# Optimization experiments

Measured on AMD Instinct MI355X. Metric: run time of the kernel, lower is better.

The kernel has to match this reference:

```python
import jax, jax.numpy as jnp
import numpy as np

EPS = 1e-5  # BatchNorm2d default eps
HEAD_DIM = 64


def conv1x1_bn_silu(x, w, gamma, beta, mean, var):
    # x: [B, Cin, H, W], w: [Cout, Cin] (1x1 conv, no bias)
    y = jnp.einsum('oc,bchw->bohw', w, x)
    scale = (gamma / jnp.sqrt(var + EPS))[None, :, None, None]
    shift = (beta - mean * gamma / jnp.sqrt(var + EPS))[None, :, None, None]
    y = y * scale + shift
    return y * jax.nn.sigmoid(y)  # SiLU


def setup_inputs() -> dict:
    key = jax.random.key(0)
    ks = jax.random.split(key, 11)
    B, C, H, W = 4, 256, 64, 64
    C3 = 3 * C
    return {
        'x': jax.random.normal(ks[0], (B, C, H, W), jnp.float32),
        'qkv_w': jax.random.normal(ks[1], (C3, C), jnp.float32) * (1.0 / np.sqrt(C)),
        'qkv_gamma': jax.random.uniform(ks[2], (C3,), jnp.float32, 0.5, 1.5),
        'qkv_beta': jax.random.normal(ks[3], (C3,), jnp.float32) * 0.1,
        'qkv_mean': jax.random.normal(ks[4], (C3,), jnp.float32) * 0.1,
        'qkv_var': jax.random.uniform(ks[5], (C3,), jnp.float32, 0.5, 1.5),
        'proj_w': jax.random.normal(ks[6], (C, C), jnp.float32) * (1.0 / np.sqrt(C)),
        'proj_gamma': jax.random.uniform(ks[7], (C,), jnp.float32, 0.5, 1.5),
        'proj_beta': jax.random.normal(ks[8], (C,), jnp.float32) * 0.1,
        'proj_mean': jax.random.normal(ks[9], (C,), jnp.float32) * 0.1,
        'proj_var': jax.random.uniform(ks[10], (C,), jnp.float32, 0.5, 1.5),
    }


def reference(x, qkv_w, qkv_gamma, qkv_beta, qkv_mean, qkv_var,
              proj_w, proj_gamma, proj_beta, proj_mean, proj_var):
    B, C, H, W = x.shape
    hd = HEAD_DIM
    nh = C // hd
    scale = hd ** -0.5

    qkv = conv1x1_bn_silu(x, qkv_w, qkv_gamma, qkv_beta, qkv_mean, qkv_var)
    # [B, 3C, H, W] -> [B, 3, nh, hd, HW] -> (3, B, nh, HW, hd)
    qkv = qkv.reshape(B, 3, nh, hd, H * W).transpose(1, 0, 2, 4, 3)
    q, k, v = qkv[0], qkv[1], qkv[2]  # each [B, nh, HW, hd]

    attn = jnp.einsum('bhqd,bhkd->bhqk', q, k) * scale
    attn = jax.nn.softmax(attn, axis=-1)
    out = jnp.einsum('bhqk,bhkd->bhqd', attn, v)  # [B, nh, HW, hd]
    out = out.transpose(0, 1, 3, 2).reshape(B, C, H, W)

    return conv1x1_bn_silu(out, proj_w, proj_gamma, proj_beta, proj_mean, proj_var)
```

## Files before the change

kernel.cpp:

```cpp
#include <hip/hip_runtime.h>
#include <hip/hip_bf16.h>
#include <math.h>

#define SLEN 4096
#define CIN 256
#define C3 768
#define NH 4
#define HD 64
#define BATCH 4

typedef __attribute__((ext_vector_type(8))) short bf16x8;
typedef __attribute__((ext_vector_type(4))) float f32x4;
typedef __attribute__((ext_vector_type(16))) float f32x16;

__device__ __forceinline__ short f2bf(float f) {
    union { float f; unsigned u; } v; v.f = f;
    unsigned r = v.u + 0x7fff + ((v.u >> 16) & 1);
    return (short)(r >> 16);
}

__device__ __forceinline__ unsigned cvt_pk(float lo, float hi) {
    unsigned r;
    asm("v_cvt_pk_bf16_f32 %0, %1, %2" : "=v"(r) : "v"(lo), "v"(hi));
    return r;
}

__global__ void k_convert_w(const float* __restrict__ qkvw, const float* __restrict__ projw,
                            short* __restrict__ qkvw_bf, short* __restrict__ projw_bf) {
    int i = blockIdx.x * 256 + threadIdx.x;
    if (i < C3 * CIN) qkvw_bf[i] = f2bf(qkvw[i]);
    if (i < CIN * CIN) projw_bf[i] = f2bf(projw[i]);
}

__global__ void k_transpose_x(const float* __restrict__ x, short* __restrict__ xT) {
    __shared__ float t[32][33];
    int b = blockIdx.z;
    int c0 = blockIdx.y * 32, s0 = blockIdx.x * 32;
    int tid = threadIdx.x;
    int r = tid >> 3, c4 = (tid & 7) * 4;
    const float* src = x + ((size_t)b * CIN + c0 + r) * SLEN + s0 + c4;
    float4 v = *reinterpret_cast<const float4*>(src);
    t[r][c4 + 0] = v.x; t[r][c4 + 1] = v.y; t[r][c4 + 2] = v.z; t[r][c4 + 3] = v.w;
    __syncthreads();
    int s_r = tid >> 3, cc = (tid & 7) * 4;
    short4 o = make_short4(f2bf(t[cc + 0][s_r]), f2bf(t[cc + 1][s_r]),
                           f2bf(t[cc + 2][s_r]), f2bf(t[cc + 3][s_r]));
    *reinterpret_cast<short4*>(xT + ((size_t)b * SLEN + s0 + s_r) * CIN + c0 + cc) = o;
}

__launch_bounds__(256)
__global__ void k_qkv(const short* __restrict__ xT, const short* __restrict__ wbf,
                      const float* __restrict__ g, const float* __restrict__ be,
                      const float* __restrict__ mu, const float* __restrict__ va,
                      short* __restrict__ Q, short* __restrict__ Kb, short* __restrict__ Vt) {
    int wv = threadIdx.x >> 6, l = threadIdx.x & 63, lr = l & 15, lg = l >> 4;
    int b = blockIdx.z;
    int s0 = blockIdx.x * 128 + wv * 32;
    int o0 = blockIdx.y * 64;
    f32x4 acc[2][4] = {};
    const short* aptr = xT + ((size_t)b * SLEN + s0 + lr) * CIN + lg * 8;
    const short* bptr = wbf + (size_t)(o0 + lr) * CIN + lg * 8;
#pragma unroll
    for (int k0 = 0; k0 < CIN; k0 += 32) {
        bf16x8 a0 = *(const bf16x8*)(aptr + k0);
        bf16x8 a1 = *(const bf16x8*)(aptr + 16 * CIN + k0);
#pragma unroll
        for (int oj = 0; oj < 4; oj++) {
            bf16x8 bb = *(const bf16x8*)(bptr + oj * 16 * CIN + k0);
            acc[0][oj] = __builtin_amdgcn_mfma_f32_16x16x32_bf16(a0, bb, acc[0][oj], 0, 0, 0);
            acc[1][oj] = __builtin_amdgcn_mfma_f32_16x16x32_bf16(a1, bb, acc[1][oj], 0, 0, 0);
        }
    }
    int which = o0 >> 8;
    int h = (o0 & 255) >> 6;
    int bh = b * NH + h;
    const float QSC = 0.125f * 1.44269504088896f;
#pragma unroll
    for (int oj = 0; oj < 4; oj++) {
        int o = o0 + oj * 16 + lr;
        float sc = g[o] * rsqrtf(va[o] + 1e-5f);
        float sh = be[o] - mu[o] * sc;
        int d = o & 63;
#pragma unroll
        for (int qi = 0; qi < 2; qi++) {
#pragma unroll
            for (int i = 0; i < 4; i++) {
                float y = acc[qi][oj][i] * sc + sh;
                float z = y / (1.f + __expf(-y));
                int s = s0 + qi * 16 + lg * 4 + i;
                if (which == 0) {
                    Q[((size_t)bh * SLEN + s) * HD + d] = f2bf(z * QSC);
                } else if (which == 1) {
                    Kb[((size_t)bh * SLEN + s) * HD + d] = f2bf(z);
                } else {
                    Vt[((size_t)bh * HD + d) * SLEN + s] = f2bf(z);
                }
            }
        }
    }
}

__launch_bounds__(256)
__global__ void k_attn(const short* __restrict__ Q, const short* __restrict__ Kg,
                       const short* __restrict__ Vg, short* __restrict__ aout) {
    __shared__ __align__(16) short klds[2][64][64];
    __shared__ __align__(16) short vlds[2][64][64];
    int tid = threadIdx.x;
    int wv = tid >> 6, l = tid & 63;
    int q32 = l & 31;
    int hi  = l >> 5;
    int bh = blockIdx.y;
    int q0 = blockIdx.x * 128 + wv * 32;

    const short* kg = Kg + (size_t)bh * SLEN * HD;
    const short* vg = Vg + (size_t)bh * HD * SLEN;

    bf16x8 qf[4];
    {
        const short* qb = Q + ((size_t)bh * SLEN + q0 + q32) * HD + hi * 8;
        qf[0] = *(const bf16x8*)(qb);
        qf[1] = *(const bf16x8*)(qb + 16);
        qf[2] = *(const bf16x8*)(qb + 32);
        qf[3] = *(const bf16x8*)(qb + 48);
    }

    bf16x8 ones;
#pragma unroll
    for (int e = 0; e < 8; ++e) ones[e] = (short)0x3F80;

    f32x16 oacc0 = {}, oacc1 = {}, sacc = {};
    float mrun = -1e30f;

    int srow = wv * 16 + (l >> 3);
    int gs = l & 7;
    int swcol = (gs ^ (l >> 3)) * 8;
    int4 rK0, rK1, rV0, rV1;

#define LOADREG(t) do { \
    const short* kgt = kg + ((size_t)(t) * 64 + srow) * HD + gs * 8; \
    rK0 = *(const int4*)(kgt); \
    rK1 = *(const int4*)(kgt + 8 * HD); \
    const short* vgt = vg + (size_t)srow * SLEN + (t) * 64 + gs * 8; \
    rV0 = *(const int4*)(vgt); \
    rV1 = *(const int4*)(vgt + 8 * SLEN); \
} while (0)

#define WRITELDS(bufb) do { \
    *(int4*)(&klds[bufb][srow][swcol]) = rK0; \
    *(int4*)(&klds[bufb][srow + 8][swcol]) = rK1; \
    *(int4*)(&vlds[bufb][srow][swcol]) = rV0; \
    *(int4*)(&vlds[bufb][srow + 8][swcol]) = rV1; \
} while (0)

#define BAR() do { asm volatile("" ::: "memory"); __builtin_amdgcn_s_barrier(); asm volatile("" ::: "memory"); } while (0)

    LOADREG(0);
    WRITELDS(0);
    LOADREG(1);
    asm volatile("s_waitcnt lgkmcnt(0)" ::: "memory");
    BAR();

    const int swz = (l & 7) << 4;

    for (int t = 0; t < SLEN / 64; ++t) {
        if (t < SLEN / 64 - 1) {
            WRITELDS((t + 1) & 1);
            if (t + 2 < SLEN / 64) LOADREG(t + 2);
        }

        const short* kb = &klds[t & 1][0][0];
        const short* vb = &vlds[t & 1][0][0];
        const short* krow0 = kb + q32 * 64;
        const short* krow1 = kb + (32 + q32) * 64;

        f32x16 s0v = {}, s1v = {};
#pragma unroll
        for (int jd = 0; jd < 4; ++jd) {
            int col = ((jd * 32 + hi * 16) ^ swz) >> 1;
            bf16x8 k0 = *(const bf16x8*)(krow0 + col);
            bf16x8 k1 = *(const bf16x8*)(krow1 + col);
            s0v = __builtin_amdgcn_mfma_f32_32x32x16_bf16(k0, qf[jd], s0v, 0, 0, 0);
            s1v = __builtin_amdgcn_mfma_f32_32x32x16_bf16(k1, qf[jd], s1v, 0, 0, 0);
        }

        float pm = fmaxf(s0v[0], s0v[1]);
#pragma unroll
        for (int r = 2; r < 16; r += 2) pm = fmaxf(pm, fmaxf(s0v[r], s0v[r + 1]));
#pragma unroll
        for (int r = 0; r < 16; r += 2) pm = fmaxf(pm, fmaxf(s1v[r], s1v[r + 1]));
        pm = fmaxf(pm, __shfl_xor(pm, 32));

        if (!__all(pm <= mrun + 10.0f)) {
            float mn = fmaxf(mrun, pm);
            float al = __builtin_amdgcn_exp2f(mrun - mn);
            mrun = mn;
#pragma unroll
            for (int r = 0; r < 16; ++r) { oacc0[r] *= al; oacc1[r] *= al; }
            sacc[0] *= al;
        }

#pragma unroll
        for (int r = 0; r < 16; ++r) {
            s0v[r] = __builtin_amdgcn_exp2f(s0v[r] - mrun);
            s1v[r] = __builtin_amdgcn_exp2f(s1v[r] - mrun);
        }

        const short* vrow0 = vb + q32 * 64;
        const short* vrow1 = vb + (32 + q32) * 64;
#pragma unroll
        for (int kc = 0; kc < 4; ++kc) {
            const f32x16& sv = (kc < 2) ? s0v : s1v;
            const int base = (kc & 1) * 8;
            unsigned A0 = cvt_pk(sv[base + 0], sv[base + 1]);
            unsigned A1 = cvt_pk(sv[base + 2], sv[base + 3]);
            unsigned A2 = cvt_pk(sv[base + 4], sv[base + 5]);
            unsigned A3 = cvt_pk(sv[base + 6], sv[base + 7]);
            asm volatile("v_permlane32_swap_b32 %0, %1" : "+v"(A0), "+v"(A2));
            asm volatile("v_permlane32_swap_b32 %0, %1" : "+v"(A1), "+v"(A3));
            union { bf16x8 v; unsigned u[4]; } pf;
            pf.u[0] = A0; pf.u[1] = A1; pf.u[2] = A2; pf.u[3] = A3;
            int col = ((kc * 32 + hi * 16) ^ swz) >> 1;
            bf16x8 v0 = *(const bf16x8*)(vrow0 + col);
            bf16x8 v1 = *(const bf16x8*)(vrow1 + col);
            oacc0 = __builtin_amdgcn_mfma_f32_32x32x16_bf16(v0, pf.v, oacc0, 0, 0, 0);
            oacc1 = __builtin_amdgcn_mfma_f32_32x32x16_bf16(v1, pf.v, oacc1, 0, 0, 0);
            sacc  = __builtin_amdgcn_mfma_f32_32x32x16_bf16(ones, pf.v, sacc, 0, 0, 0);
        }

        if (t < SLEN / 64 - 1) {
            asm volatile("s_waitcnt lgkmcnt(0)" ::: "memory");
            BAR();
        }
    }

    float inv = 1.f / sacc[0];
    int b = bh >> 2, h = bh & 3;
    short* ob = aout + ((size_t)b * SLEN + q0 + q32) * CIN + h * HD;
#pragma unroll
    for (int g4 = 0; g4 < 4; ++g4) {
        uint2 st0, st1;
        st0.x = cvt_pk(oacc0[4 * g4 + 0] * inv, oacc0[4 * g4 + 1] * inv);
        st0.y = cvt_pk(oacc0[4 * g4 + 2] * inv, oacc0[4 * g4 + 3] * inv);
        st1.x = cvt_pk(oacc1[4 * g4 + 0] * inv, oacc1[4 * g4 + 1] * inv);
        st1.y = cvt_pk(oacc1[4 * g4 + 2] * inv, oacc1[4 * g4 + 3] * inv);
        *(uint2*)(ob + 8 * g4 + 4 * hi) = st0;
        *(uint2*)(ob + 32 + 8 * g4 + 4 * hi) = st1;
    }
#undef LOADREG
#undef WRITELDS
#undef BAR
}

__launch_bounds__(256)
__global__ void k_proj(const short* __restrict__ aout, const short* __restrict__ wbf,
                       const float* __restrict__ g, const float* __restrict__ be,
                       const float* __restrict__ mu, const float* __restrict__ va,
                       float* __restrict__ out) {
    int wv = threadIdx.x >> 6, l = threadIdx.x & 63, lr = l & 15, lg = l >> 4;
    int b = blockIdx.z;
    int s0 = blockIdx.x * 128 + wv * 32;
    int o0 = blockIdx.y * 64;
    f32x4 acc[2][4] = {};
    const short* aptr = aout + ((size_t)b * SLEN + s0 + lr) * CIN + lg * 8;
    const short* bptr = wbf + (size_t)(o0 + lr) * CIN + lg * 8;
#pragma unroll
    for (int k0 = 0; k0 < CIN; k0 += 32) {
        bf16x8 a0 = *(const bf16x8*)(aptr + k0);
        bf16x8 a1 = *(const bf16x8*)(aptr + 16 * CIN + k0);
#pragma unroll
        for (int oj = 0; oj < 4; oj++) {
            bf16x8 bb = *(const bf16x8*)(bptr + oj * 16 * CIN + k0);
            acc[0][oj] = __builtin_amdgcn_mfma_f32_16x16x32_bf16(a0, bb, acc[0][oj], 0, 0, 0);
            acc[1][oj] = __builtin_amdgcn_mfma_f32_16x16x32_bf16(a1, bb, acc[1][oj], 0, 0, 0);
        }
    }
#pragma unroll
    for (int oj = 0; oj < 4; oj++) {
        int o = o0 + oj * 16 + lr;
        float sc = g[o] * rsqrtf(va[o] + 1e-5f);
        float sh = be[o] - mu[o] * sc;
#pragma unroll
        for (int qi = 0; qi < 2; qi++) {
            float4 st;
            float* stp = &st.x;
#pragma unroll
            for (int i = 0; i < 4; i++) {
                float y = acc[qi][oj][i] * sc + sh;
                stp[i] = y / (1.f + __expf(-y));
            }
            int s = s0 + qi * 16 + lg * 4;
            *reinterpret_cast<float4*>(out + ((size_t)b * CIN + o) * SLEN + s) = st;
        }
    }
}

extern "C" void kernel_launch(void* const* d_in, const int* in_sizes, int n_in,
                              void* d_out, int out_size, void* d_ws, size_t ws_size,
                              hipStream_t stream) {
    const float* x    = (const float*)d_in[0];
    const float* qkvw = (const float*)d_in[1];
    const float* qg   = (const float*)d_in[2];
    const float* qbe  = (const float*)d_in[3];
    const float* qmu  = (const float*)d_in[4];
    const float* qva  = (const float*)d_in[5];
    const float* pw   = (const float*)d_in[6];
    const float* pg   = (const float*)d_in[7];
    const float* pbe  = (const float*)d_in[8];
    const float* pmu  = (const float*)d_in[9];
    const float* pva  = (const float*)d_in[10];
    float* out = (float*)d_out;

    char* ws = (char*)d_ws;
    short* xT       = (short*)(ws);
    short* qkvw_bf  = (short*)(ws + 8388608);
    short* projw_bf = (short*)(ws + 8781824);
    short* Qb       = (short*)(ws + 8912896);
    short* Kb       = (short*)(ws + 17301504);
    short* Vt       = (short*)(ws + 25690112);
    short* aout     = (short*)(ws + 34078720);

    k_convert_w<<<768, 256, 0, stream>>>(qkvw, pw, qkvw_bf, projw_bf);
    k_transpose_x<<<dim3(128, 8, 4), 256, 0, stream>>>(x, xT);
    k_qkv<<<dim3(32, 12, 4), 256, 0, stream>>>(xT, qkvw_bf, qg, qbe, qmu, qva, Qb, Kb, Vt);
    k_attn<<<dim3(32, 16), 256, 0, stream>>>(Qb, Kb, Vt, aout);
    k_proj<<<dim3(32, 4, 4), 256, 0, stream>>>(aout, projw_bf, pg, pbe, pmu, pva, out);
}
```

Baseline: 173.4 us.

## Software-pipeline attention: overlap next tile's QK^T with current softmax/PV

Restructures the attention main loop so the QK^T MFMAs for tile t+1 are issued alongside the softmax and PV step for tile t, with ping-pong score registers and a 2x-unrolled loop. V gets a triple LDS buffer so the V tile being consumed stays valid while the next one is written. The intent is to hide softmax and exp latency behind matrix-core work. It also adds a launch bound of 2 blocks per SM and a tree-shaped max reduction. The extra live score registers raise VGPR pressure and could cause spills under the occupancy bound.

```diff
diff --git a/kernel.cpp b/kernel.cpp
--- a/kernel.cpp
+++ b/kernel.cpp
@@ -100,11 +100,11 @@
     }
 }
 
-__launch_bounds__(256)
+__launch_bounds__(256, 2)
 __global__ void k_attn(const short* __restrict__ Q, const short* __restrict__ Kg,
                        const short* __restrict__ Vg, short* __restrict__ aout) {
     __shared__ __align__(16) short klds[2][64][64];
-    __shared__ __align__(16) short vlds[2][64][64];
+    __shared__ __align__(16) short vlds[3][64][64];
     int tid = threadIdx.x;
     int wv = tid >> 6, l = tid & 63;
     int q32 = l & 31;
@@ -145,49 +145,43 @@
     rV1 = *(const int4*)(vgt + 8 * SLEN); \
 } while (0)
 
-#define WRITELDS(bufb) do { \
-    *(int4*)(&klds[bufb][srow][swcol]) = rK0; \
-    *(int4*)(&klds[bufb][srow + 8][swcol]) = rK1; \
-    *(int4*)(&vlds[bufb][srow][swcol]) = rV0; \
-    *(int4*)(&vlds[bufb][srow + 8][swcol]) = rV1; \
+#define WRITELDS(kbuf, vbuf) do { \
+    *(int4*)(&klds[kbuf][srow][swcol]) = rK0; \
+    *(int4*)(&klds[kbuf][srow + 8][swcol]) = rK1; \
+    *(int4*)(&vlds[vbuf][srow][swcol]) = rV0; \
+    *(int4*)(&vlds[vbuf][srow + 8][swcol]) = rV1; \
 } while (0)
 
 #define BAR() do { asm volatile("" ::: "memory"); __builtin_amdgcn_s_barrier(); asm volatile("" ::: "memory"); } while (0)
-
-    LOADREG(0);
-    WRITELDS(0);
-    LOADREG(1);
-    asm volatile("s_waitcnt lgkmcnt(0)" ::: "memory");
-    BAR();
+#define WAITBAR() do { asm volatile("s_waitcnt lgkmcnt(0)" ::: "memory"); BAR(); } while (0)
 
     const int swz = (l & 7) << 4;
 
-    for (int t = 0; t < SLEN / 64; ++t) {
-        if (t < SLEN / 64 - 1) {
-            WRITELDS((t + 1) & 1);
-            if (t + 2 < SLEN / 64) LOADREG(t + 2);
-        }
-
+    auto qk = [&](int t, f32x16& d0, f32x16& d1) {
         const short* kb = &klds[t & 1][0][0];
-        const short* vb = &vlds[t & 1][0][0];
         const short* krow0 = kb + q32 * 64;
         const short* krow1 = kb + (32 + q32) * 64;
-
-        f32x16 s0v = {}, s1v = {};
+        d0 = (f32x16){}; d1 = (f32x16){};
 #pragma unroll
         for (int jd = 0; jd < 4; ++jd) {
             int col = ((jd * 32 + hi * 16) ^ swz) >> 1;
             bf16x8 k0 = *(const bf16x8*)(krow0 + col);
             bf16x8 k1 = *(const bf16x8*)(krow1 + col);
-            s0v = __builtin_amdgcn_mfma_f32_32x32x16_bf16(k0, qf[jd], s0v, 0, 0, 0);
-            s1v = __builtin_amdgcn_mfma_f32_32x32x16_bf16(k1, qf[jd], s1v, 0, 0, 0);
-        }
-
-        float pm = fmaxf(s0v[0], s0v[1]);
-#pragma unroll
-        for (int r = 2; r < 16; r += 2) pm = fmaxf(pm, fmaxf(s0v[r], s0v[r + 1]));
-#pragma unroll
-        for (int r = 0; r < 16; r += 2) pm = fmaxf(pm, fmaxf(s1v[r], s1v[r + 1]));
+            d0 = __builtin_amdgcn_mfma_f32_32x32x16_bf16(k0, qf[jd], d0, 0, 0, 0);
+            d1 = __builtin_amdgcn_mfma_f32_32x32x16_bf16(k1, qf[jd], d1, 0, 0, 0);
+        }
+    };
+
+    auto smpv = [&](int tt, f32x16& s0v, f32x16& s1v) {
+        float pa = fmaxf(fmaxf(fmaxf(s0v[0], s0v[1]), fmaxf(s0v[2], s0v[3])),
+                         fmaxf(fmaxf(s0v[4], s0v[5]), fmaxf(s0v[6], s0v[7])));
+        float pb = fmaxf(fmaxf(fmaxf(s0v[8], s0v[9]), fmaxf(s0v[10], s0v[11])),
+                         fmaxf(fmaxf(s0v[12], s0v[13]), fmaxf(s0v[14], s0v[15])));
+        float pc = fmaxf(fmaxf(fmaxf(s1v[0], s1v[1]), fmaxf(s1v[2], s1v[3])),
+                         fmaxf(fmaxf(s1v[4], s1v[5]), fmaxf(s1v[6], s1v[7])));
+        float pd = fmaxf(fmaxf(fmaxf(s1v[8], s1v[9]), fmaxf(s1v[10], s1v[11])),
+                         fmaxf(fmaxf(s1v[12], s1v[13]), fmaxf(s1v[14], s1v[15])));
+        float pm = fmaxf(fmaxf(pa, pb), fmaxf(pc, pd));
         pm = fmaxf(pm, __shfl_xor(pm, 32));
 
         if (!__all(pm <= mrun + 10.0f)) {
@@ -205,6 +199,7 @@
             s1v[r] = __builtin_amdgcn_exp2f(s1v[r] - mrun);
         }
 
+        const short* vb = &vlds[tt % 3][0][0];
         const short* vrow0 = vb + q32 * 64;
         const short* vrow1 = vb + (32 + q32) * 64;
 #pragma unroll
@@ -226,12 +221,36 @@
             oacc1 = __builtin_amdgcn_mfma_f32_32x32x16_bf16(v1, pf.v, oacc1, 0, 0, 0);
             sacc  = __builtin_amdgcn_mfma_f32_32x32x16_bf16(ones, pf.v, sacc, 0, 0, 0);
         }
-
-        if (t < SLEN / 64 - 1) {
-            asm volatile("s_waitcnt lgkmcnt(0)" ::: "memory");
-            BAR();
-        }
-    }
+    };
+
+    f32x16 sA0, sA1, sB0, sB1;
+
+    LOADREG(0);
+    WRITELDS(0, 0);
+    LOADREG(1);
+    WAITBAR();
+
+    WRITELDS(1, 1);
+    LOADREG(2);
+    qk(0, sA0, sA1);
+    WAITBAR();
+
+    for (int t = 1; t < 63; t += 2) {
+        WRITELDS((t + 1) & 1, (t + 1) % 3);
+        LOADREG(t + 2);
+        qk(t, sB0, sB1);
+        smpv(t - 1, sA0, sA1);
+        WAITBAR();
+        WRITELDS((t + 2) & 1, (t + 2) % 3);
+        if (t + 3 < 64) LOADREG(t + 3);
+        qk(t + 1, sA0, sA1);
+        smpv(t, sB0, sB1);
+        WAITBAR();
+    }
+
+    qk(63, sB0, sB1);
+    smpv(62, sA0, sA1);
+    smpv(63, sB0, sB1);
 
     float inv = 1.f / sacc[0];
     int b = bh >> 2, h = bh & 3;
@@ -249,6 +268,7 @@
 #undef LOADREG
 #undef WRITELDS
 #undef BAR
+#undef WAITBAR
 }
 
 __launch_bounds__(256)
```

Measured after the change: 167.5 us. -3.4%, faster.

## Software-pipeline QK^T and softmax/PV across tiles with deeper V buffering

Applied to the files above, without the earlier changes.

Restructures the attention loop so the QK^T MFMAs for the next key tile are issued while the current tile's softmax and PV run, using two score register sets and a manually unrolled four-stage schedule. V gets four LDS buffers and K two, and scores are initialised with the negated running max so the subtraction folds into the MFMA accumulator. When the max has not changed, a fast path skips that subtraction. It also requests two blocks per CU via launch bounds. The cost is higher register pressure and more LDS per block, which may limit occupancy.

```diff
diff --git a/kernel.cpp b/kernel.cpp
--- a/kernel.cpp
+++ b/kernel.cpp
@@ -100,11 +100,10 @@
     }
 }
 
-__launch_bounds__(256)
+__launch_bounds__(256, 2)
 __global__ void k_attn(const short* __restrict__ Q, const short* __restrict__ Kg,
                        const short* __restrict__ Vg, short* __restrict__ aout) {
-    __shared__ __align__(16) short klds[2][64][64];
-    __shared__ __align__(16) short vlds[2][64][64];
+    __shared__ __align__(16) char lds[16384 + 32768];
     int tid = threadIdx.x;
     int wv = tid >> 6, l = tid & 63;
     int q32 = l & 31;
@@ -129,109 +128,141 @@
     for (int e = 0; e < 8; ++e) ones[e] = (short)0x3F80;
 
     f32x16 oacc0 = {}, oacc1 = {}, sacc = {};
-    float mrun = -1e30f;
+    float mrun = 0.0f, bA = 0.0f, bB = 0.0f;
 
     int srow = wv * 16 + (l >> 3);
     int gs = l & 7;
-    int swcol = (gs ^ (l >> 3)) * 8;
+    int swz = (l & 7) << 4;
+    int soff = srow * 128 + ((gs ^ (l >> 3)) << 4);
+    int a0 = q32 * 128 + ((0 * 32 + hi * 16) ^ swz);
+    int a1 = q32 * 128 + ((1 * 32 + hi * 16) ^ swz);
+    int a2 = q32 * 128 + ((2 * 32 + hi * 16) ^ swz);
+    int a3 = q32 * 128 + ((3 * 32 + hi * 16) ^ swz);
+
+    int klane = srow * HD + gs * 8;
+    int vlane = srow * SLEN + gs * 8;
     int4 rK0, rK1, rV0, rV1;
 
-#define LOADREG(t) do { \
-    const short* kgt = kg + ((size_t)(t) * 64 + srow) * HD + gs * 8; \
+#define LOADREG(T) do { \
+    const short* kgt = kg + (size_t)(T) * 4096 + klane; \
     rK0 = *(const int4*)(kgt); \
     rK1 = *(const int4*)(kgt + 8 * HD); \
-    const short* vgt = vg + (size_t)srow * SLEN + (t) * 64 + gs * 8; \
+    const short* vgt = vg + (size_t)(T) * 64 + vlane; \
     rV0 = *(const int4*)(vgt); \
     rV1 = *(const int4*)(vgt + 8 * SLEN); \
 } while (0)
 
-#define WRITELDS(bufb) do { \
-    *(int4*)(&klds[bufb][srow][swcol]) = rK0; \
-    *(int4*)(&klds[bufb][srow + 8][swcol]) = rK1; \
-    *(int4*)(&vlds[bufb][srow][swcol]) = rV0; \
-    *(int4*)(&vlds[bufb][srow + 8][swcol]) = rV1; \
+#define WRITELDS(KB, VB) do { \
+    *(int4*)(lds + soff + (KB) * 8192) = rK0; \
+    *(int4*)(lds + soff + (KB) * 8192 + 1024) = rK1; \
+    *(int4*)(lds + soff + 16384 + (VB) * 8192) = rV0; \
+    *(int4*)(lds + soff + 16384 + (VB) * 8192 + 1024) = rV1; \
 } while (0)
 
 #define BAR() do { asm volatile("" ::: "memory"); __builtin_amdgcn_s_barrier(); asm volatile("" ::: "memory"); } while (0)
+#define WAITBAR() do { asm volatile("s_waitcnt lgkmcnt(0)" ::: "memory"); BAR(); } while (0)
+
+#define MFMA32(A, B, C) __builtin_amdgcn_mfma_f32_32x32x16_bf16(A, B, C)
+
+#define QKT(KB, D0, D1, BSET) do { \
+    BSET = mrun; \
+    float nb_ = -mrun; \
+    _Pragma("unroll") for (int r_ = 0; r_ < 16; ++r_) { D0[r_] = nb_; D1[r_] = nb_; } \
+    { \
+        bf16x8 k0_, k1_; \
+        k0_ = *(const bf16x8*)(lds + a0 + (KB) * 8192); \
+        k1_ = *(const bf16x8*)(lds + a0 + (KB) * 8192 + 4096); \
+        D0 = __builtin_amdgcn_mfma_f32_32x32x16_bf16(k0_, qf[0], D0, 0, 0, 0); \
+        D1 = __builtin_amdgcn_mfma_f32_32x32x16_bf16(k1_, qf[0], D1, 0, 0, 0); \
+        k0_ = *(const bf16x8*)(lds + a1 + (KB) * 8192); \
+        k1_ = *(const bf16x8*)(lds + a1 + (KB) * 8192 + 4096); \
+        D0 = __builtin_amdgcn_mfma_f32_32x32x16_bf16(k0_, qf[1], D0, 0, 0, 0); \
+        D1 = __builtin_amdgcn_mfma_f32_32x32x16_bf16(k1_, qf[1], D1, 0, 0, 0); \
+        k0_ = *(const bf16x8*)(lds + a2 + (KB) * 8192); \
+        k1_ = *(const bf16x8*)(lds + a2 + (KB) * 8192 + 4096); \
+        D0 = __builtin_amdgcn_mfma_f32_32x32x16_bf16(k0_, qf[2], D0, 0, 0, 0); \
+        D1 = __builtin_amdgcn_mfma_f32_32x32x16_bf16(k1_, qf[2], D1, 0, 0, 0); \
+        k0_ = *(const bf16x8*)(lds + a3 + (KB) * 8192); \
+        k1_ = *(const bf16x8*)(lds + a3 + (KB) * 8192 + 4096); \
+        D0 = __builtin_amdgcn_mfma_f32_32x32x16_bf16(k0_, qf[3], D0, 0, 0, 0); \
+        D1 = __builtin_amdgcn_mfma_f32_32x32x16_bf16(k1_, qf[3], D1, 0, 0, 0); \
+    } \
+} while (0)
+
+#define PVKC(AK, SV, BASE, VB) do { \
+    unsigned A0_ = cvt_pk(SV[(BASE) + 0], SV[(BASE) + 1]); \
+    unsigned A1_ = cvt_pk(SV[(BASE) + 2], SV[(BASE) + 3]); \
+    unsigned A2_ = cvt_pk(SV[(BASE) + 4], SV[(BASE) + 5]); \
+    unsigned A3_ = cvt_pk(SV[(BASE) + 6], SV[(BASE) + 7]); \
+    asm volatile("v_permlane32_swap_b32 %0, %1" : "+v"(A0_), "+v"(A2_)); \
+    asm volatile("v_permlane32_swap_b32 %0, %1" : "+v"(A1_), "+v"(A3_)); \
+    union { bf16x8 v; unsigned u[4]; } pf_; \
+    pf_.u[0] = A0_; pf_.u[1] = A1_; pf_.u[2] = A2_; pf_.u[3] = A3_; \
+    bf16x8 v0_ = *(const bf16x8*)(lds + (AK) + 16384 + (VB) * 8192); \
+    bf16x8 v1_ = *(const bf16x8*)(lds + (AK) + 16384 + (VB) * 8192 + 4096); \
+    oacc0 = __builtin_amdgcn_mfma_f32_32x32x16_bf16(v0_, pf_.v, oacc0, 0, 0, 0); \
+    oacc1 = __builtin_amdgcn_mfma_f32_32x32x16_bf16(v1_, pf_.v, oacc1, 0, 0, 0); \
+    sacc  = __builtin_amdgcn_mfma_f32_32x32x16_bf16(ones, pf_.v, sacc, 0, 0, 0); \
+} while (0)
+
+#define SMPV(VB, S0, S1, BSET) do { \
+    float pa_ = S0[0], pb_ = S0[8], pc_ = S1[0], pd_ = S1[8]; \
+    _Pragma("unroll") for (int r_ = 1; r_ < 8; ++r_) { \
+        pa_ = fmaxf(pa_, S0[r_]); pb_ = fmaxf(pb_, S0[8 + r_]); \
+        pc_ = fmaxf(pc_, S1[r_]); pd_ = fmaxf(pd_, S1[8 + r_]); \
+    } \
+    float pms_ = fmaxf(fmaxf(pa_, pb_), fmaxf(pc_, pd_)); \
+    float c1_ = pms_, c2_ = pms_; \
+    asm volatile("" : "+v"(c2_));  \
+    asm volatile("v_permlane32_swap_b32 %0, %1" : "+v"(c1_), "+v"(c2_)); \
+    pms_ = fmaxf(c1_, c2_); \
+    float db_ = mrun - (BSET); \
+    if (!__all(pms_ <= db_ + 10.0f)) { \
+        float mn_ = fmaxf(mrun, pms_ + (BSET)); \
+        float al_ = __builtin_amdgcn_exp2f(mrun - mn_); \
+        _Pragma("unroll") for (int r_ = 0; r_ < 16; ++r_) { oacc0[r_] *= al_; oacc1[r_] *= al_; } \
+        sacc[0] *= al_; \
+        mrun = mn_; db_ = mn_ - (BSET); \
+    } \
+    if (__all(db_ == 0.0f)) { \
+        _Pragma("unroll") for (int r_ = 0; r_ < 16; ++r_) { \
+            S0[r_] = __builtin_amdgcn_exp2f(S0[r_]); \
+            S1[r_] = __builtin_amdgcn_exp2f(S1[r_]); \
+        } \
+    } else { \
+        _Pragma("unroll") for (int r_ = 0; r_ < 16; ++r_) { \
+            S0[r_] = __builtin_amdgcn_exp2f(S0[r_] - db_); \
+            S1[r_] = __builtin_amdgcn_exp2f(S1[r_] - db_); \
+        } \
+    } \
+    PVKC(a0, S0, 0, VB); \
+    PVKC(a1, S0, 8, VB); \
+    PVKC(a2, S1, 0, VB); \
+    PVKC(a3, S1, 8, VB); \
+} while (0)
+
+    f32x16 sA0, sA1, sB0, sB1;
 
     LOADREG(0);
-    WRITELDS(0);
+    WRITELDS(0, 0);
     LOADREG(1);
-    asm volatile("s_waitcnt lgkmcnt(0)" ::: "memory");
-    BAR();
-
-    const int swz = (l & 7) << 4;
-
-    for (int t = 0; t < SLEN / 64; ++t) {
-        if (t < SLEN / 64 - 1) {
-            WRITELDS((t + 1) & 1);
-            if (t + 2 < SLEN / 64) LOADREG(t + 2);
-        }
-
-        const short* kb = &klds[t & 1][0][0];
-        const short* vb = &vlds[t & 1][0][0];
-        const short* krow0 = kb + q32 * 64;
-        const short* krow1 = kb + (32 + q32) * 64;
-
-        f32x16 s0v = {}, s1v = {};
-#pragma unroll
-        for (int jd = 0; jd < 4; ++jd) {
-            int col = ((jd * 32 + hi * 16) ^ swz) >> 1;
-            bf16x8 k0 = *(const bf16x8*)(krow0 + col);
-            bf16x8 k1 = *(const bf16x8*)(krow1 + col);
-            s0v = __builtin_amdgcn_mfma_f32_32x32x16_bf16(k0, qf[jd], s0v, 0, 0, 0);
-            s1v = __builtin_amdgcn_mfma_f32_32x32x16_bf16(k1, qf[jd], s1v, 0, 0, 0);
-        }
-
-        float pm = fmaxf(s0v[0], s0v[1]);
-#pragma unroll
-        for (int r = 2; r < 16; r += 2) pm = fmaxf(pm, fmaxf(s0v[r], s0v[r + 1]));
-#pragma unroll
-        for (int r = 0; r < 16; r += 2) pm = fmaxf(pm, fmaxf(s1v[r], s1v[r + 1]));
-        pm = fmaxf(pm, __shfl_xor(pm, 32));
-
-        if (!__all(pm <= mrun + 10.0f)) {
-            float mn = fmaxf(mrun, pm);
-            float al = __builtin_amdgcn_exp2f(mrun - mn);
-            mrun = mn;
-#pragma unroll
-            for (int r = 0; r < 16; ++r) { oacc0[r] *= al; oacc1[r] *= al; }
-            sacc[0] *= al;
-        }
-
-#pragma unroll
-        for (int r = 0; r < 16; ++r) {
-            s0v[r] = __builtin_amdgcn_exp2f(s0v[r] - mrun);
-            s1v[r] = __builtin_amdgcn_exp2f(s1v[r] - mrun);
-        }
-
-        const short* vrow0 = vb + q32 * 64;
-        const short* vrow1 = vb + (32 + q32) * 64;
-#pragma unroll
-        for (int kc = 0; kc < 4; ++kc) {
-            const f32x16& sv = (kc < 2) ? s0v : s1v;
-            const int base = (kc & 1) * 8;
-            unsigned A0 = cvt_pk(sv[base + 0], sv[base + 1]);
-            unsigned A1 = cvt_pk(sv[base + 2], sv[base + 3]);
-            unsigned A2 = cvt_pk(sv[base + 4], sv[base + 5]);
-            unsigned A3 = cvt_pk(sv[base + 6], sv[base + 7]);
-            asm volatile("v_permlane32_swap_b32 %0, %1" : "+v"(A0), "+v"(A2));
-            asm volatile("v_permlane32_swap_b32 %0, %1" : "+v"(A1), "+v"(A3));
-            union { bf16x8 v; unsigned u[4]; } pf;
-            pf.u[0] = A0; pf.u[1] = A1; pf.u[2] = A2; pf.u[3] = A3;
-            int col = ((kc * 32 + hi * 16) ^ swz) >> 1;
-            bf16x8 v0 = *(const bf16x8*)(vrow0 + col);
-            bf16x8 v1 = *(const bf16x8*)(vrow1 + col);
-            oacc0 = __builtin_amdgcn_mfma_f32_32x32x16_bf16(v0, pf.v, oacc0, 0, 0, 0);
-            oacc1 = __builtin_amdgcn_mfma_f32_32x32x16_bf16(v1, pf.v, oacc1, 0, 0, 0);
-            sacc  = __builtin_amdgcn_mfma_f32_32x32x16_bf16(ones, pf.v, sacc, 0, 0, 0);
-        }
-
-        if (t < SLEN / 64 - 1) {
-            asm volatile("s_waitcnt lgkmcnt(0)" ::: "memory");
-            BAR();
-        }
-    }
+    WAITBAR();
+    WRITELDS(1, 1);
+    LOADREG(2);
+    QKT(0, sA0, sA1, bA);
+    WAITBAR();
+
+    for (int j = 0; j < 15; ++j) {
+        int t = 4 * j + 1;
+        WRITELDS(0, 2); LOADREG(t + 2); QKT(1, sB0, sB1, bB); SMPV(0, sA0, sA1, bA); WAITBAR();
+        WRITELDS(1, 3); LOADREG(t + 3); QKT(0, sA0, sA1, bA); SMPV(1, sB0, sB1, bB); WAITBAR();
+        WRITELDS(0, 0); LOADREG(t + 4); QKT(1, sB0, sB1, bB); SMPV(2, sA0, sA1, bA); WAITBAR();
+        WRITELDS(1, 1); LOADREG(t + 5); QKT(0, sA0, sA1, bA); SMPV(3, sB0, sB1, bB); WAITBAR();
+    }
+    WRITELDS(0, 2); LOADREG(63); QKT(1, sB0, sB1, bB); SMPV(0, sA0, sA1, bA); WAITBAR();
+    WRITELDS(1, 3); QKT(0, sA0, sA1, bA); SMPV(1, sB0, sB1, bB); WAITBAR();
+    QKT(1, sB0, sB1, bB); SMPV(2, sA0, sA1, bA);
+    SMPV(3, sB0, sB1, bB);
 
     float inv = 1.f / sacc[0];
     int b = bh >> 2, h = bh & 3;
@@ -249,6 +280,11 @@
 #undef LOADREG
 #undef WRITELDS
 #undef BAR
+#undef WAITBAR
+#undef MFMA32
+#undef QKT
+#undef PVKC
+#undef SMPV
 }
 
 __launch_bounds__(256)
```

Result: faster. 163.5 us (-5.7%).
